# Kernel tuning notes

Measured on AMD Instinct MI355X. Metric: run time of the kernel, lower is better.

Reference implementation:

```python
import jax, jax.numpy as jnp
import numpy as np

B, DIM, HEADS, H, W = 8, 128, 8, 128, 128
EPS_NORM = 1e-12
BN_EPS = 1e-5


def _conv(x, w, b=None, pad=0, groups=1):
    # x: [N,C,H,W], w: [O, C//groups, kh, kw]
    out = jax.lax.conv_general_dilated(
        x, w, window_strides=(1, 1), padding=[(pad, pad), (pad, pad)],
        dimension_numbers=('NCHW', 'OIHW', 'NCHW'), feature_group_count=groups)
    if b is not None:
        out = out + b[None, :, None, None]
    return out


def _l2norm_lastdim(t):
    # torch F.normalize(dim=-1) semantics; works for real or complex t
    n = jnp.sqrt(jnp.sum(jnp.abs(t) ** 2, axis=-1, keepdims=True))
    return t / jnp.maximum(n, EPS_NORM)


def setup_inputs() -> dict:
    key = jax.random.key(0)
    ks = iter(jax.random.split(key, 48))
    d = DIM

    def rn(shape, scale=0.02):
        return jax.random.normal(next(ks), shape, jnp.float32) * scale

    inp = {
        'x': jax.random.normal(next(ks), (B, d, H, W), jnp.float32),
        # ---- Attention_F params ----
        'temp_f': jnp.ones((HEADS, 1, 1), jnp.float32),
        'w1': rn((d // 16, d, 1, 1)), 'b1': jnp.zeros((d // 16,), jnp.float32),
        'bn_gamma': jnp.ones((d // 16,), jnp.float32), 'bn_beta': jnp.zeros((d // 16,), jnp.float32),
        'bn_mean': jnp.zeros((d // 16,), jnp.float32), 'bn_var': jnp.ones((d // 16,), jnp.float32),
        'w2': rn((d, d // 16, 1, 1)), 'b2': jnp.zeros((d,), jnp.float32),
        'projf_w': rn((d, 2 * d, 1, 1)),
        # ---- Attention_S params ----
        'temp_s': jnp.ones((HEADS, 1, 1), jnp.float32),
        'q1_w': rn((d, d, 1, 1)), 'q1_b': jnp.zeros((d,), jnp.float32),
        'k1_w': rn((d, d, 1, 1)), 'k1_b': jnp.zeros((d,), jnp.float32),
        'v1_w': rn((d, d, 1, 1)), 'v1_b': jnp.zeros((d,), jnp.float32),
        'q3_w': rn((d // 2, 2, 3, 3)), 'q5_w': rn((d // 2, 2, 5, 5)),
        'k3_w': rn((d // 2, 2, 3, 3)), 'k5_w': rn((d // 2, 2, 5, 5)),
        'v3_w': rn((d // 2, 2, 3, 3)), 'v5_w': rn((d // 2, 2, 5, 5)),
        'c3_w': rn((d // 2, 2, 3, 3)), 'c5_w': rn((d // 2, 2, 5, 5)),
        'projs_w': rn((d, 2 * d, 1, 1)),
    }
    return inp


def _fssa(x, temp_f, w1, b1, bn_gamma, bn_beta, bn_mean, bn_var, w2, b2, projf_w,
          temp_s, q1_w, q1_b, k1_w, k1_b, v1_w, v1_b,
          q3_w, q5_w, k3_w, k5_w, v3_w, v5_w, c3_w, c5_w, projs_w):
    b, c, h, w = x.shape
    hd = c // HEADS
    groups = c // 2  # grouped convs: dim -> dim//2, 2 in-ch per group

    # ================= Attention_F (frequency branch) =================
    xf = jnp.fft.fft2(x)                     # [b,c,h,w] complex; q=k=v=fft2(x)
    qf = xf.reshape(b, HEADS, hd, h * w)
    qn = _l2norm_lastdim(qf)
    # attn: [b,head,hd,hd] complex, temperature is real [head,1,1]
    attn_f = jnp.einsum('bhcn,bhdn->bhcd', qn, qn) * temp_f[None]
    # complex softmax: softmax real & imag parts separately
    attn_f = jax.lax.complex(jax.nn.softmax(attn_f.real, axis=-1),
                             jax.nn.softmax(attn_f.imag, axis=-1))
    out_cplx = jnp.einsum('bhcd,bhdn->bhcn', attn_f, qf)
    # NOTE: torch.fft.ifft2 acts on the LAST TWO dims of [b,head,hd,hw]
    out_f = jnp.abs(jnp.fft.ifft2(out_cplx)).reshape(b, c, h, w)

    # SE-style gate in frequency domain on the real part
    g = _conv(xf.real, w1, b1)
    g = (g - bn_mean[None, :, None, None]) / jnp.sqrt(bn_var[None, :, None, None] + BN_EPS)
    g = g * bn_gamma[None, :, None, None] + bn_beta[None, :, None, None]
    g = jax.nn.relu(g)
    g = jax.nn.sigmoid(_conv(g, w2, b2))     # [b,c,h,w] real gate
    out_f_l = jnp.abs(jnp.fft.ifft2(g * xf))  # ifft2 over (h,w)

    fsa = _conv(jnp.concatenate([out_f, out_f_l], axis=1), projf_w)

    # ================= Attention_S (spatial branch) =================
    def qkv(w1x1, b1x1, w3, w5):
        t = _conv(x, w1x1, b1x1)
        return jnp.concatenate([_conv(t, w3, pad=1, groups=groups),
                                _conv(t, w5, pad=2, groups=groups)], axis=1)

    q_s = qkv(q1_w, q1_b, q3_w, q5_w).reshape(b, HEADS, hd, h * w)
    k_s = qkv(k1_w, k1_b, k3_w, k5_w).reshape(b, HEADS, hd, h * w)
    v_s = qkv(v1_w, v1_b, v3_w, v5_w).reshape(b, HEADS, hd, h * w)
    q_s = _l2norm_lastdim(q_s)
    k_s = _l2norm_lastdim(k_s)
    attn_s = jnp.einsum('bhcn,bhdn->bhcd', q_s, k_s) * temp_s[None]
    attn_s = jax.nn.softmax(attn_s, axis=-1)
    out_s = jnp.einsum('bhcd,bhdn->bhcn', attn_s, v_s).reshape(b, c, h, w)

    out_s_l = jnp.concatenate([_conv(x, c3_w, pad=1, groups=groups),
                               _conv(x, c5_w, pad=2, groups=groups)], axis=1)
    ssa = _conv(jnp.concatenate([out_s, out_s_l], axis=1), projs_w)

    return fsa + ssa


def reference(x, temp_f, w1, b1, bn_gamma, bn_beta, bn_mean, bn_var, w2, b2, projf_w,
              temp_s, q1_w, q1_b, k1_w, k1_b, v1_w, v1_b,
              q3_w, q5_w, k3_w, k5_w, v3_w, v5_w, c3_w, c5_w, projs_w):
    return _fssa(x, temp_f, w1, b1, bn_gamma, bn_beta, bn_mean, bn_var, w2, b2, projf_w,
                 temp_s, q1_w, q1_b, k1_w, k1_b, v1_w, v1_b,
                 q3_w, q5_w, k3_w, k5_w, v3_w, v5_w, c3_w, c5_w, projs_w)
```

## Files before the change

### kernel.cpp

```cpp
#include <hip/hip_runtime.h>
#include <math.h>

#define B 8
#define C 128
#define HEADS 8
#define HD 16
#define HH 128
#define WW 128
#define P 16384

static __device__ __forceinline__ float PI2F() { return 6.28318530717958647692f; }

template<int SIGN, bool GATE>
__global__ __launch_bounds__(256) void k_fftcol(
        const float* __restrict__ inR, const float* __restrict__ inI,
        const float* __restrict__ Mg, const float* __restrict__ w2,
        const float* __restrict__ b2,
        float* __restrict__ outR, float* __restrict__ outI) {
    __shared__ float2 S[128*32];
    __shared__ float2 tw[64];
    int bid = blockIdx.x;
    int img = bid >> 2;
    int qo  = (bid & 3) * 32;
    int tid = threadIdx.x;
    if (tid < 64) {
        float a = PI2F() * (float)tid / 128.0f;
        float s_, c_; __sincosf(a, &s_, &c_);
        tw[tid] = make_float2(c_, SIGN > 0 ? s_ : -s_);
    }
    long base = (long)img * P;
    float w2r[8]; float b2c = 0.f;
    const float* mb = nullptr;
    if (GATE) {
        int c = img & 127;
        #pragma unroll
        for (int j = 0; j < 8; ++j) w2r[j] = w2[c*8 + j];
        b2c = b2[c];
        mb = Mg + (long)(img >> 7)*8*P;
    }
    #pragma unroll
    for (int t = 0; t < 16; ++t) {
        int idx = tid + t*256;
        int h = idx >> 5, cc = idx & 31;
        int off = h*128 + qo + cc;
        float xr = inR[base + off];
        float xi = inI[base + off];
        if (GATE) {
            float z = b2c;
            #pragma unroll
            for (int j = 0; j < 8; ++j) z = fmaf(w2r[j], mb[(long)j*P + off], z);
            float g = 1.0f / (1.0f + __expf(-z));
            xr *= g; xi *= g;
        }
        int hr = __brev(h) >> 25;
        S[hr*32 + cc] = make_float2(xr, xi);
    }
    __syncthreads();
    int ln = tid & 31, wid = tid >> 5;
    for (int s = 0; s < 7; ++s) {
        int half = 1 << s;
        #pragma unroll
        for (int q = 0; q < 8; ++q) {
            int j = wid*8 + q;
            int k = j & (half - 1);
            int g = j >> s;
            int i0 = (g << (s+1)) + k;
            int i1 = i0 + half;
            float2 u = S[i0*32 + ln];
            float2 v = S[i1*32 + ln];
            float2 w = tw[k << (6 - s)];
            float vr = v.x*w.x - v.y*w.y;
            float vi = v.x*w.y + v.y*w.x;
            S[i0*32 + ln] = make_float2(u.x + vr, u.y + vi);
            S[i1*32 + ln] = make_float2(u.x - vr, u.y - vi);
        }
        __syncthreads();
    }
    #pragma unroll
    for (int t = 0; t < 16; ++t) {
        int idx = tid + t*256;
        int k = idx >> 5, cc = idx & 31;
        float2 z = S[k*32 + cc];
        outR[base + k*128 + qo + cc] = z.x;
        outI[base + k*128 + qo + cc] = z.y;
    }
}

template<int MODE>
__global__ __launch_bounds__(256) void k_fftrow(
        const float* __restrict__ inR, const float* __restrict__ inI,
        float* __restrict__ out, float* __restrict__ outI) {
    __shared__ float2 S[4*128];
    __shared__ float2 tw[64];
    int bid = blockIdx.x;
    int img = bid >> 5;
    int r0  = (bid & 31) * 4;
    int tid = threadIdx.x;
    if (tid < 64) {
        float a = PI2F() * (float)tid / 128.0f;
        float s_, c_; __sincosf(a, &s_, &c_);
        tw[tid] = make_float2(c_, MODE == 0 ? -s_ : s_);
    }
    long base = (long)img * P;
    #pragma unroll
    for (int t = 0; t < 2; ++t) {
        int idx = tid + t*256;
        int r = idx >> 7, w = idx & 127;
        long off = base + (long)(r0 + r)*128 + w;
        float xr = inR[off];
        float xi = (MODE == 0) ? 0.f : inI[off];
        if (MODE == 2) {
            int k2 = r0 + r;
            float ang = (PI2F()/16384.0f) * (float)(w * k2);
            float s_, c_; __sincosf(ang, &s_, &c_);
            float yr = xr*c_ - xi*s_;
            float yi = xr*s_ + xi*c_;
            xr = yr; xi = yi;
        }
        S[r*128 + (__brev(w) >> 25)] = make_float2(xr, xi);
    }
    __syncthreads();
    int r = tid >> 6, j = tid & 63;
    for (int s = 0; s < 7; ++s) {
        int half = 1 << s;
        int k = j & (half - 1);
        int g = j >> s;
        int i0 = (g << (s+1)) + k;
        int i1 = i0 + half;
        float2 u = S[r*128 + i0];
        float2 v = S[r*128 + i1];
        float2 w_ = tw[k << (6 - s)];
        float vr = v.x*w_.x - v.y*w_.y;
        float vi = v.x*w_.y + v.y*w_.x;
        S[r*128 + i0] = make_float2(u.x + vr, u.y + vi);
        S[r*128 + i1] = make_float2(u.x - vr, u.y - vi);
        __syncthreads();
    }
    if (MODE == 0) {
        #pragma unroll
        for (int t = 0; t < 2; ++t) {
            int idx = tid + t*256;
            int rr = idx >> 7, k = idx & 127;
            float2 z = S[rr*128 + k];
            long off = base + (long)(r0 + rr)*128 + k;
            out[off] = z.x; outI[off] = z.y;
        }
    } else if (MODE == 1) {
        #pragma unroll
        for (int t = 0; t < 2; ++t) {
            int idx = tid + t*256;
            int rr = idx >> 7, p = idx & 127;
            float2 z = S[rr*128 + p];
            out[base + (long)(r0 + rr)*128 + p] =
                sqrtf(z.x*z.x + z.y*z.y) * (1.0f/16384.0f);
        }
    } else {
        if (tid < 128) {
            int k1 = tid;
            float4 v;
            float2 z0 = S[0*128 + k1], z1 = S[1*128 + k1];
            float2 z2 = S[2*128 + k1], z3 = S[3*128 + k1];
            v.x = sqrtf(z0.x*z0.x + z0.y*z0.y) * (1.0f/16384.0f);
            v.y = sqrtf(z1.x*z1.x + z1.y*z1.y) * (1.0f/16384.0f);
            v.z = sqrtf(z2.x*z2.x + z2.y*z2.y) * (1.0f/16384.0f);
            v.w = sqrtf(z3.x*z3.x + z3.y*z3.y) * (1.0f/16384.0f);
            *(float4*)(out + base + (long)k1*128 + r0) = v;
        }
    }
}

__global__ __launch_bounds__(256) void k_gate_mid(
        const float* __restrict__ XFr, const float* __restrict__ w1,
        const float* __restrict__ b1, const float* __restrict__ gamma,
        const float* __restrict__ beta, const float* __restrict__ mean,
        const float* __restrict__ var, float* __restrict__ M) {
    __shared__ float w1s[8*128];
    int tid = threadIdx.x;
    for (int i = tid; i < 1024; i += 256) w1s[i] = w1[i];
    __syncthreads();
    int tile = blockIdx.x;
    int b = tile >> 4;
    long pbase = (long)(tile & 15)*1024 + tid*4;
    const float4* xp = (const float4*)(XFr + (long)b*C*P + pbase);
    float4 acc[8];
    #pragma unroll
    for (int j = 0; j < 8; ++j) { float bj = b1[j]; acc[j] = make_float4(bj,bj,bj,bj); }
    for (int c = 0; c < 128; ++c) {
        float4 xv = xp[c*(P/4)];
        #pragma unroll
        for (int j = 0; j < 8; ++j) {
            float w = w1s[j*128 + c];
            acc[j].x = fmaf(w, xv.x, acc[j].x);
            acc[j].y = fmaf(w, xv.y, acc[j].y);
            acc[j].z = fmaf(w, xv.z, acc[j].z);
            acc[j].w = fmaf(w, xv.w, acc[j].w);
        }
    }
    #pragma unroll
    for (int j = 0; j < 8; ++j) {
        float sc = rsqrtf(var[j] + 1e-5f) * gamma[j];
        float sh = beta[j] - mean[j]*sc;
        float4 v;
        v.x = fmaxf(fmaf(acc[j].x, sc, sh), 0.f);
        v.y = fmaxf(fmaf(acc[j].y, sc, sh), 0.f);
        v.z = fmaxf(fmaf(acc[j].z, sc, sh), 0.f);
        v.w = fmaxf(fmaf(acc[j].w, sc, sh), 0.f);
        *(float4*)(M + ((long)b*8 + j)*P + pbase) = v;
    }
}

__global__ __launch_bounds__(256) void k_gram_cr(
        const float* __restrict__ Xr, const float* __restrict__ Xi,
        float* __restrict__ gramP, float* __restrict__ normP) {
    __shared__ float Sr[16][260];
    __shared__ float Si[16][260];
    int bh = blockIdx.x >> 3, ck = blockIdx.x & 7;
    int tid = threadIdx.x;
    int tile = tid & 15;
    int slice = tid >> 4;
    int ci4 = (tile >> 2) * 4, di4 = (tile & 3) * 4;
    long rowb = (long)bh * 16;
    int n0 = ck * 2048;
    float acc[4][4];
    #pragma unroll
    for (int a = 0; a < 4; ++a)
        #pragma unroll
        for (int b2 = 0; b2 < 4; ++b2) acc[a][b2] = 0.f;
    float nacc = 0.f;
    int nrow = tid & 15;
    int ngrp = tid >> 4;
    for (int sc = 0; sc < 8; ++sc) {
        int nb = n0 + sc*256;
        if (sc) __syncthreads();
        for (int i = tid; i < 1024; i += 256) {
            int r = i >> 6, col = (i & 63) * 4;
            *(float4*)(&Sr[r][col]) = *(const float4*)(Xr + (rowb + r)*P + nb + col);
            *(float4*)(&Si[r][col]) = *(const float4*)(Xi + (rowb + r)*P + nb + col);
        }
        __syncthreads();
        #pragma unroll
        for (int it0 = 0; it0 < 4; ++it0) {
            int it = (it0 + slice) & 3;
            int n = slice*16 + it*4;
            float4 cr[4], cii[4], dr[4], dii[4];
            #pragma unroll
            for (int a = 0; a < 4; ++a) {
                cr[a]  = *(const float4*)(&Sr[ci4 + a][n]);
                cii[a] = *(const float4*)(&Si[ci4 + a][n]);
                dr[a]  = *(const float4*)(&Sr[di4 + a][n]);
                dii[a] = *(const float4*)(&Si[di4 + a][n]);
            }
            #pragma unroll
            for (int a = 0; a < 4; ++a)
                #pragma unroll
                for (int b2 = 0; b2 < 4; ++b2) {
                    float t = acc[a][b2];
                    t = fmaf(cr[a].x, dr[b2].x, fmaf(-cii[a].x, dii[b2].x, t));
                    t = fmaf(cr[a].y, dr[b2].y, fmaf(-cii[a].y, dii[b2].y, t));
                    t = fmaf(cr[a].z, dr[b2].z, fmaf(-cii[a].z, dii[b2].z, t));
                    t = fmaf(cr[a].w, dr[b2].w, fmaf(-cii[a].w, dii[b2].w, t));
                    acc[a][b2] = t;
                }
        }
        #pragma unroll
        for (int it0 = 0; it0 < 4; ++it0) {
            int it = (it0 + ngrp) & 3;
            int n = ngrp*16 + it*4;
            float4 r4 = *(const float4*)(&Sr[nrow][n]);
            float4 i4 = *(const float4*)(&Si[nrow][n]);
            nacc = fmaf(r4.x, r4.x, fmaf(i4.x, i4.x, nacc));
            nacc = fmaf(r4.y, r4.y, fmaf(i4.y, i4.y, nacc));
            nacc = fmaf(r4.z, r4.z, fmaf(i4.z, i4.z, nacc));
            nacc = fmaf(r4.w, r4.w, fmaf(i4.w, i4.w, nacc));
        }
    }
    __syncthreads();
    float* red  = &Sr[0][0];
    float* redn = &Si[0][0];
    #pragma unroll
    for (int a = 0; a < 4; ++a)
        #pragma unroll
        for (int b2 = 0; b2 < 4; ++b2)
            red[tile*256 + slice*16 + a*4 + b2] = acc[a][b2];
    redn[nrow*16 + ngrp] = nacc;
    __syncthreads();
    {
        int c = tid >> 4, d = tid & 15;
        int tI = (c >> 2)*4 + (d >> 2);
        int lo = (c & 3)*4 + (d & 3);
        float g = 0.f;
        #pragma unroll
        for (int s = 0; s < 16; ++s) g += red[tI*256 + s*16 + lo];
        gramP[(long)(bh*8 + ck)*256 + tid] = g;
    }
    if (tid < 16) {
        float s = 0.f;
        #pragma unroll
        for (int k = 0; k < 16; ++k) s += redn[tid*16 + k];
        normP[(long)(bh*8 + ck)*16 + tid] = s;
    }
}

__global__ __launch_bounds__(256) void k_gram_r(
        const float* __restrict__ Q, const float* __restrict__ K,
        float* __restrict__ gramP, float* __restrict__ qnormP,
        float* __restrict__ knormP) {
    __shared__ float Sq[16][260];
    __shared__ float Sk[16][260];
    int bh = blockIdx.x >> 3, ck = blockIdx.x & 7;
    int tid = threadIdx.x;
    int tile = tid & 15;
    int slice = tid >> 4;
    int ci4 = (tile >> 2) * 4, di4 = (tile & 3) * 4;
    long rowb = (long)bh * 16;
    int n0 = ck * 2048;
    float acc[4][4];
    #pragma unroll
    for (int a = 0; a < 4; ++a)
        #pragma unroll
        for (int b2 = 0; b2 < 4; ++b2) acc[a][b2] = 0.f;
    float qacc = 0.f, kacc = 0.f;
    int nrow = tid & 15, ngrp = tid >> 4;
    for (int sc = 0; sc < 8; ++sc) {
        int nb = n0 + sc*256;
        if (sc) __syncthreads();
        for (int i = tid; i < 1024; i += 256) {
            int r = i >> 6, col = (i & 63) * 4;
            *(float4*)(&Sq[r][col]) = *(const float4*)(Q + (rowb + r)*P + nb + col);
            *(float4*)(&Sk[r][col]) = *(const float4*)(K + (rowb + r)*P + nb + col);
        }
        __syncthreads();
        #pragma unroll
        for (int it0 = 0; it0 < 4; ++it0) {
            int it = (it0 + slice) & 3;
            int n = slice*16 + it*4;
            float4 cq[4], dk[4];
            #pragma unroll
            for (int a = 0; a < 4; ++a) {
                cq[a] = *(const float4*)(&Sq[ci4 + a][n]);
                dk[a] = *(const float4*)(&Sk[di4 + a][n]);
            }
            #pragma unroll
            for (int a = 0; a < 4; ++a)
                #pragma unroll
                for (int b2 = 0; b2 < 4; ++b2) {
                    float t = acc[a][b2];
                    t = fmaf(cq[a].x, dk[b2].x, t);
                    t = fmaf(cq[a].y, dk[b2].y, t);
                    t = fmaf(cq[a].z, dk[b2].z, t);
                    t = fmaf(cq[a].w, dk[b2].w, t);
                    acc[a][b2] = t;
                }
        }
        #pragma unroll
        for (int it0 = 0; it0 < 4; ++it0) {
            int it = (it0 + ngrp) & 3;
            int n = ngrp*16 + it*4;
            float4 q4 = *(const float4*)(&Sq[nrow][n]);
            float4 k4 = *(const float4*)(&Sk[nrow][n]);
            qacc = fmaf(q4.x, q4.x, qacc); kacc = fmaf(k4.x, k4.x, kacc);
            qacc = fmaf(q4.y, q4.y, qacc); kacc = fmaf(k4.y, k4.y, kacc);
            qacc = fmaf(q4.z, q4.z, qacc); kacc = fmaf(k4.z, k4.z, kacc);
            qacc = fmaf(q4.w, q4.w, qacc); kacc = fmaf(k4.w, k4.w, kacc);
        }
    }
    __syncthreads();
    float* red  = &Sq[0][0];
    float* redn = &Sk[0][0];
    #pragma unroll
    for (int a = 0; a < 4; ++a)
        #pragma unroll
        for (int b2 = 0; b2 < 4; ++b2)
            red[tile*256 + slice*16 + a*4 + b2] = acc[a][b2];
    redn[nrow*16 + ngrp] = qacc;
    redn[256 + nrow*16 + ngrp] = kacc;
    __syncthreads();
    {
        int c = tid >> 4, d = tid & 15;
        int tI = (c >> 2)*4 + (d >> 2);
        int lo = (c & 3)*4 + (d & 3);
        float g = 0.f;
        #pragma unroll
        for (int s = 0; s < 16; ++s) g += red[tI*256 + s*16 + lo];
        gramP[(long)(bh*8 + ck)*256 + tid] = g;
    }
    if (tid < 16) {
        float s = 0.f;
        #pragma unroll
        for (int k = 0; k < 16; ++k) s += redn[tid*16 + k];
        qnormP[(long)(bh*8 + ck)*16 + tid] = s;
    } else if (tid < 32) {
        int r = tid - 16;
        float s = 0.f;
        #pragma unroll
        for (int k = 0; k < 16; ++k) s += redn[256 + r*16 + k];
        knormP[(long)(bh*8 + ck)*16 + r] = s;
    }
}

__global__ void k_attn_f(const float* __restrict__ gramP, const float* __restrict__ normP,
                         const float* __restrict__ tempf, float* __restrict__ attn2) {
    int bh = blockIdx.x; int tid = threadIdx.x;
    int c = tid >> 4, d = tid & 15;
    int hh = bh & 7;
    __shared__ float sR[256];
    __shared__ float2 t16[16];
    __shared__ float sN[16];
    if (tid < 16) {
        float s = 0.f;
        #pragma unroll
        for (int ck = 0; ck < 8; ++ck) s += normP[(long)(bh*8+ck)*16 + tid];
        sN[tid] = 1.0f / fmaxf(sqrtf(s), 1e-12f);
        float a = PI2F() * (float)tid / 16.0f;
        t16[tid] = make_float2(__cosf(a), __sinf(a));
    }
    float gr = 0.f;
    for (int ck = 0; ck < 8; ++ck) gr += gramP[(long)(bh*8+ck)*256 + tid];
    __syncthreads();
    float vr = gr * sN[c] * sN[d] * tempf[hh];
    float mr = vr;
    for (int off = 8; off >= 1; off >>= 1) mr = fmaxf(mr, __shfl_xor(mr, off));
    float er = __expf(vr - mr);
    float ssr = er;
    for (int off = 8; off >= 1; off >>= 1) ssr += __shfl_xor(ssr, off);
    float arv = er / ssr;
    const float u = 1.0f/16.0f;
    sR[tid] = arv;
    __syncthreads();
    float ar2 = 0.f, ai2 = 0.f;
    #pragma unroll
    for (int cc = 0; cc < 16; ++cc) {
        float2 t = t16[(cc*c) & 15];
        float xr = sR[cc*16 + d];
        ar2 = fmaf(xr, t.x, fmaf(-u, t.y, ar2));
        ai2 = fmaf(xr, t.y, fmaf( u, t.x, ai2));
    }
    long o = ((long)bh*256 + tid)*2;
    attn2[o]   = ar2 * (1.0f/16.0f);
    attn2[o+1] = ai2 * (1.0f/16.0f);
}

__global__ void k_yf(const float* __restrict__ attn2, const float* __restrict__ Xr,
                     const float* __restrict__ Xi, float* __restrict__ Yr,
                     float* __restrict__ Yi) {
    int bh = blockIdx.x >> 6;
    int nb = blockIdx.x & 63;
    int tid = threadIdx.x;
    __shared__ float aR[256], aI[256];
    { long o = ((long)bh*256 + tid)*2; aR[tid] = attn2[o]; aI[tid] = attn2[o+1]; }
    __syncthreads();
    long n = (long)nb*256 + tid;
    long rowb = (long)bh*16;
    float qr[16], qi[16];
    #pragma unroll
    for (int dd = 0; dd < 16; ++dd) {
        qr[dd] = Xr[(rowb+dd)*P + n];
        qi[dd] = Xi[(rowb+dd)*P + n];
    }
    for (int cc = 0; cc < 16; ++cc) {
        float ar = 0.f, ai = 0.f;
        #pragma unroll
        for (int dd = 0; dd < 16; ++dd) {
            float tr = aR[cc*16+dd], ti = aI[cc*16+dd];
            ar = fmaf(tr, qr[dd], fmaf(-ti, qi[dd], ar));
            ai = fmaf(tr, qi[dd], fmaf( ti, qr[dd], ai));
        }
        Yr[(rowb+cc)*P + n] = ar;
        Yi[(rowb+cc)*P + n] = ai;
    }
}

__global__ __launch_bounds__(256) void k_conv1x1qkv(
        const float* __restrict__ x,
        const float* __restrict__ Wq, const float* __restrict__ bq,
        const float* __restrict__ Wk, const float* __restrict__ bk,
        const float* __restrict__ Wv, const float* __restrict__ bv,
        float* __restrict__ Oq, float* __restrict__ Ok,
        float* __restrict__ Ov) {
    __shared__ float Ws[16*128];
    int og = blockIdx.y & 7, which = blockIdx.y >> 3;
    int b = blockIdx.z;
    const float* W    = which == 0 ? Wq : which == 1 ? Wk : Wv;
    const float* bias = which == 0 ? bq : which == 1 ? bk : bv;
    float* O          = which == 0 ? Oq : which == 1 ? Ok : Ov;
    int tid = threadIdx.x;
    for (int i = tid; i < 2048; i += 256) Ws[i] = W[og*2048 + i];
    __syncthreads();
    long pbase = (long)blockIdx.x*1024 + tid*4;
    const float4* xp = (const float4*)(x + (long)b*C*P + pbase);
    float4 acc[16];
    #pragma unroll
    for (int j = 0; j < 16; ++j) { float bj = bias[og*16+j]; acc[j] = make_float4(bj,bj,bj,bj); }
    for (int c = 0; c < 128; ++c) {
        float4 xv = xp[c*(P/4)];
        #pragma unroll
        for (int j = 0; j < 16; ++j) {
            float w = Ws[j*128 + c];
            acc[j].x = fmaf(w, xv.x, acc[j].x);
            acc[j].y = fmaf(w, xv.y, acc[j].y);
            acc[j].z = fmaf(w, xv.z, acc[j].z);
            acc[j].w = fmaf(w, xv.w, acc[j].w);
        }
    }
    float* op = O + (long)b*C*P + (long)og*16*P + pbase;
    #pragma unroll
    for (int j = 0; j < 16; ++j) *(float4*)(op + (long)j*P) = acc[j];
}

__global__ __launch_bounds__(256) void k_gconv(
        const float* __restrict__ in, const float* __restrict__ w3,
        const float* __restrict__ w5, float* __restrict__ out) {
    __shared__ float S[2*20*132];
    __shared__ float ws3[18], ws5[50];
    int ht = blockIdx.x;
    int g  = blockIdx.y;
    int b  = blockIdx.z;
    int tid = threadIdx.x;
    int h0 = ht*16;
    const float* ib = in + ((long)b*C + 2*g)*P;
    if (tid < 18) ws3[tid] = w3[g*18 + tid];
    else if (tid < 68) ws5[tid-18] = w5[g*50 + tid - 18];
    for (int i = tid; i < 2*20*132; i += 256) {
        int ic = i / 2640, rem = i % 2640;
        int t = rem / 132, cc = rem % 132;
        int h = h0 - 2 + t, w = cc - 2;
        float v = 0.f;
        if (h >= 0 && h < 128 && w >= 0 && w < 128)
            v = ib[(long)ic*P + h*128 + w];
        S[i] = v;
    }
    __syncthreads();
    int w = tid & 127, rh = tid >> 7;
    int lr0 = rh*8;
    float acc3[8], acc5[8];
    #pragma unroll
    for (int r = 0; r < 8; ++r) { acc3[r] = 0.f; acc5[r] = 0.f; }
    #pragma unroll
    for (int ic = 0; ic < 2; ++ic) {
        const float* Sc = S + ic*2640;
        #pragma unroll
        for (int kx = 0; kx < 3; ++kx) {
            float col[10];
            #pragma unroll
            for (int i = 0; i < 10; ++i)
                col[i] = Sc[(lr0 + 1 + i)*132 + (w + 1 + kx)];
            #pragma unroll
            for (int ky = 0; ky < 3; ++ky) {
                float wv = ws3[ic*9 + ky*3 + kx];
                #pragma unroll
                for (int r = 0; r < 8; ++r)
                    acc3[r] = fmaf(wv, col[r + ky], acc3[r]);
            }
        }
        #pragma unroll
        for (int kx = 0; kx < 5; ++kx) {
            float col[12];
            #pragma unroll
            for (int i = 0; i < 12; ++i)
                col[i] = Sc[(lr0 + i)*132 + (w + kx)];
            #pragma unroll
            for (int ky = 0; ky < 5; ++ky) {
                float wv = ws5[ic*25 + ky*5 + kx];
                #pragma unroll
                for (int r = 0; r < 8; ++r)
                    acc5[r] = fmaf(wv, col[r + ky], acc5[r]);
            }
        }
    }
    long ob3 = ((long)b*C + g)*P;
    long ob5 = ((long)b*C + 64 + g)*P;
    #pragma unroll
    for (int r = 0; r < 8; ++r) {
        int h = h0 + lr0 + r;
        out[ob3 + h*128 + w] = acc3[r];
        out[ob5 + h*128 + w] = acc5[r];
    }
}

__global__ void k_attn_s(const float* __restrict__ gramP, const float* __restrict__ qnormP,
                         const float* __restrict__ knormP, const float* __restrict__ temps,
                         float* __restrict__ attn) {
    int bh = blockIdx.x; int tid = threadIdx.x;
    int c = tid >> 4, d = tid & 15;
    __shared__ float sQ[16], sK[16];
    if (tid < 16) {
        float sq = 0.f, sk = 0.f;
        #pragma unroll
        for (int ck = 0; ck < 8; ++ck) {
            sq += qnormP[(long)(bh*8+ck)*16 + tid];
            sk += knormP[(long)(bh*8+ck)*16 + tid];
        }
        sQ[tid] = 1.0f / fmaxf(sqrtf(sq), 1e-12f);
        sK[tid] = 1.0f / fmaxf(sqrtf(sk), 1e-12f);
    }
    float g = 0.f;
    for (int ck = 0; ck < 8; ++ck) g += gramP[(long)(bh*8+ck)*256 + tid];
    __syncthreads();
    g *= sQ[c] * sK[d] * temps[bh & 7];
    float m = g;
    for (int off = 8; off >= 1; off >>= 1) m = fmaxf(m, __shfl_xor(m, off));
    float e = __expf(g - m);
    float s = e;
    for (int off = 8; off >= 1; off >>= 1) s += __shfl_xor(s, off);
    attn[(long)bh*256 + tid] = e / s;
}

__global__ void k_outs(const float* __restrict__ attn, const float* __restrict__ V,
                       float* __restrict__ out) {
    int bh = blockIdx.x >> 6, nb = blockIdx.x & 63;
    int tid = threadIdx.x;
    __shared__ float aS[256];
    aS[tid] = attn[(long)bh*256 + tid];
    __syncthreads();
    long n = (long)nb*256 + tid;
    long rowb = (long)bh*16;
    float vv[16];
    #pragma unroll
    for (int dd = 0; dd < 16; ++dd) vv[dd] = V[(rowb+dd)*P + n];
    for (int cc = 0; cc < 16; ++cc) {
        float a = 0.f;
        #pragma unroll
        for (int dd = 0; dd < 16; ++dd) a = fmaf(aS[cc*16+dd], vv[dd], a);
        out[(rowb+cc)*P + n] = a;
    }
}

template<bool ADD>
__global__ __launch_bounds__(256) void k_proj2in(
        const float* __restrict__ A, const float* __restrict__ Bc,
        const float* __restrict__ W, float* __restrict__ out) {
    __shared__ float Ws[16*256];
    int og = blockIdx.y, b = blockIdx.z;
    int tid = threadIdx.x;
    for (int i = tid; i < 4096; i += 256) Ws[i] = W[og*4096 + i];
    __syncthreads();
    long pbase = (long)blockIdx.x*1024 + tid*4;
    long xb = (long)b*C*P;
    const float4* Ap = (const float4*)(A + xb + pbase);
    const float4* Bp = (const float4*)(Bc + xb + pbase);
    float4 acc[16];
    #pragma unroll
    for (int j = 0; j < 16; ++j) acc[j] = make_float4(0.f,0.f,0.f,0.f);
    for (int c = 0; c < 128; ++c) {
        float4 a = Ap[c*(P/4)];
        float4 bb = Bp[c*(P/4)];
        #pragma unroll
        for (int j = 0; j < 16; ++j) {
            float w0 = Ws[j*256 + c], w1 = Ws[j*256 + 128 + c];
            acc[j].x = fmaf(w0, a.x, fmaf(w1, bb.x, acc[j].x));
            acc[j].y = fmaf(w0, a.y, fmaf(w1, bb.y, acc[j].y));
            acc[j].z = fmaf(w0, a.z, fmaf(w1, bb.z, acc[j].z));
            acc[j].w = fmaf(w0, a.w, fmaf(w1, bb.w, acc[j].w));
        }
    }
    float* op = out + xb + (long)og*16*P + pbase;
    #pragma unroll
    for (int j = 0; j < 16; ++j) {
        float4 v = acc[j];
        if (ADD) {
            float4 o = *(float4*)(op + (long)j*P);
            v.x += o.x; v.y += o.y; v.z += o.z; v.w += o.w;
        }
        *(float4*)(op + (long)j*P) = v;
    }
}

static long ws_need_bytes(int bc) {
    long pb = (long)bc * C * P;
    long extras = (long)bc*8*P
                + (long)bc*1024*3
                + (long)bc*8*8*256
                + (long)bc*8*256*2
                + (long)bc*8*8*256
                + (long)bc*8*256;
    return (5*pb + extras) * 4;
}

extern "C" void kernel_launch(void* const* d_in, const int* in_sizes, int n_in,
                              void* d_out, int out_size, void* d_ws, size_t ws_size,
                              hipStream_t stream) {
    const float* x      = (const float*)d_in[0];
    const float* temp_f = (const float*)d_in[1];
    const float* w1     = (const float*)d_in[2];
    const float* b1     = (const float*)d_in[3];
    const float* bng    = (const float*)d_in[4];
    const float* bnb    = (const float*)d_in[5];
    const float* bnm    = (const float*)d_in[6];
    const float* bnv    = (const float*)d_in[7];
    const float* w2     = (const float*)d_in[8];
    const float* b2     = (const float*)d_in[9];
    const float* projf  = (const float*)d_in[10];
    const float* temp_s = (const float*)d_in[11];
    const float* q1w = (const float*)d_in[12]; const float* q1b = (const float*)d_in[13];
    const float* k1w = (const float*)d_in[14]; const float* k1b = (const float*)d_in[15];
    const float* v1w = (const float*)d_in[16]; const float* v1b = (const float*)d_in[17];
    const float* q3w = (const float*)d_in[18]; const float* q5w = (const float*)d_in[19];
    const float* k3w = (const float*)d_in[20]; const float* k5w = (const float*)d_in[21];
    const float* v3w = (const float*)d_in[22]; const float* v5w = (const float*)d_in[23];
    const float* c3w = (const float*)d_in[24]; const float* c5w = (const float*)d_in[25];
    const float* projs  = (const float*)d_in[26];
    float* out = (float*)d_out;
    float* ws = (float*)d_ws;

    int bc = 1;
    if ((long)ws_size >= ws_need_bytes(8)) bc = 8;
    else if ((long)ws_size >= ws_need_bytes(4)) bc = 4;
    else if ((long)ws_size >= ws_need_bytes(2)) bc = 2;
    const int NB = bc;
    const long pb = (long)bc * C * P;

    float* t0 = ws + 0*pb;
    float* t1 = ws + 1*pb;
    float* t2 = ws + 2*pb;
    float* t3 = ws + 3*pb;
    float* t4 = ws + 4*pb;
    float* Mg    = ws + 5*pb;
    float* normF = Mg + (long)bc*8*P;
    float* recQ  = normF + (long)bc*1024;
    float* recK  = recQ + (long)bc*1024;
    float* gramC = recK + (long)bc*1024;
    float* attn2 = gramC + (long)bc*8*8*256;
    float* gramS = attn2 + (long)bc*8*256*2;
    float* attnS = gramS + (long)bc*8*8*256;

    for (int ckk = 0; ckk < 8/bc; ++ckk) {
        const float* xc = x + (long)ckk * bc * C * P;
        float* outc = out + (long)ckk * bc * C * P;

        k_fftrow<0><<<NB*C*32, 256, 0, stream>>>(xc, nullptr, t0, t1);
        k_fftcol<-1,false><<<NB*C*4, 256, 0, stream>>>(t0, t1, nullptr, nullptr,
                                                       nullptr, t2, t3);
        k_gate_mid<<<NB*16, 256, 0, stream>>>(t2, w1, b1, bng, bnb, bnm, bnv, Mg);
        k_fftcol<1,true><<<NB*C*4, 256, 0, stream>>>(t2, t3, Mg, w2, b2,
                                                     t0, t1);
        k_fftrow<1><<<NB*C*32, 256, 0, stream>>>(t0, t1, t4, nullptr);
        k_gram_cr<<<NB*8*8, 256, 0, stream>>>(t2, t3, gramC, normF);
        k_attn_f<<<NB*8, 256, 0, stream>>>(gramC, normF, temp_f, attn2);
        k_yf<<<NB*8*64, 256, 0, stream>>>(attn2, t2, t3, t0, t1);
        k_fftcol<1,false><<<NB*C*4, 256, 0, stream>>>(t0, t1, nullptr, nullptr,
                                                      nullptr, t2, t3);
        k_fftrow<2><<<NB*C*32, 256, 0, stream>>>(t2, t3, t0, nullptr);
        k_proj2in<false><<<dim3(16, 8, NB), 256, 0, stream>>>(t0, t4, projf, outc);

        k_conv1x1qkv<<<dim3(16, 24, NB), 256, 0, stream>>>(xc, q1w, q1b, k1w, k1b,
                                                           v1w, v1b, t0, t1, t2);
        k_gconv<<<dim3(8, 64, NB), 256, 0, stream>>>(t0, q3w, q5w, t3);
        k_gconv<<<dim3(8, 64, NB), 256, 0, stream>>>(t1, k3w, k5w, t4);
        k_gconv<<<dim3(8, 64, NB), 256, 0, stream>>>(t2, v3w, v5w, t0);
        k_gconv<<<dim3(8, 64, NB), 256, 0, stream>>>(xc, c3w, c5w, t1);
        k_gram_r<<<NB*8*8, 256, 0, stream>>>(t3, t4, gramS, recQ, recK);
        k_attn_s<<<NB*8, 256, 0, stream>>>(gramS, recQ, recK, temp_s, attnS);
        k_outs<<<NB*8*64, 256, 0, stream>>>(attnS, t0, t2);
        k_proj2in<true><<<dim3(16, 8, NB), 256, 0, stream>>>(t2, t1, projs, outc);
    }
}
```

Measured before the change: 1.627 ms.

## Retile pointwise conv kernels with transposed smem weights and prefetch

Reworks the three 1x1-conv style kernels (gate_mid, conv1x1qkv, proj2in). Weights are stored transposed in shared memory so each channel step loads them as float4 vectors instead of scalar reads. The next channel's input is loaded one iteration early. conv1x1qkv now computes q, k and v together from a single read of x, and proj2in makes 32 outputs per thread over 2 pixels instead of 16 over 4, which halves how often each input is reread. The cost is higher register pressure from 64-96 accumulators and changed grid shapes.

```diff
diff --git a/kernel.cpp b/kernel.cpp
--- a/kernel.cpp
+++ b/kernel.cpp
@@ -10,6 +10,10 @@
 #define P 16384
 
 static __device__ __forceinline__ float PI2F() { return 6.28318530717958647692f; }
+
+#define FMA4(ACC, W, X) \
+    ACC.x = fmaf(W, X.x, ACC.x); ACC.y = fmaf(W, X.y, ACC.y); \
+    ACC.z = fmaf(W, X.z, ACC.z); ACC.w = fmaf(W, X.w, ACC.w);
 
 template<int SIGN, bool GATE>
 __global__ __launch_bounds__(256) void k_fftcol(
@@ -174,38 +178,40 @@
         const float* __restrict__ b1, const float* __restrict__ gamma,
         const float* __restrict__ beta, const float* __restrict__ mean,
         const float* __restrict__ var, float* __restrict__ M) {
-    __shared__ float w1s[8*128];
-    int tid = threadIdx.x;
-    for (int i = tid; i < 1024; i += 256) w1s[i] = w1[i];
+    __shared__ float Wt[128][8];
+    int tid = threadIdx.x;
+    for (int i = tid; i < 1024; i += 256) { int c = i >> 3, j = i & 7; Wt[c][j] = w1[j*128 + c]; }
     __syncthreads();
     int tile = blockIdx.x;
-    int b = tile >> 4;
-    long pbase = (long)(tile & 15)*1024 + tid*4;
-    const float4* xp = (const float4*)(XFr + (long)b*C*P + pbase);
-    float4 acc[8];
-    #pragma unroll
-    for (int j = 0; j < 8; ++j) { float bj = b1[j]; acc[j] = make_float4(bj,bj,bj,bj); }
+    int b = tile >> 5;
+    long pbase = (long)(tile & 31)*512 + tid*2;
+    const float2* xp = (const float2*)(XFr + (long)b*C*P + pbase);
+    float2 acc[8];
+    #pragma unroll
+    for (int j = 0; j < 8; ++j) { float bj = b1[j]; acc[j] = make_float2(bj, bj); }
+    float2 xv = xp[0];
     for (int c = 0; c < 128; ++c) {
-        float4 xv = xp[c*(P/4)];
-        #pragma unroll
-        for (int j = 0; j < 8; ++j) {
-            float w = w1s[j*128 + c];
-            acc[j].x = fmaf(w, xv.x, acc[j].x);
-            acc[j].y = fmaf(w, xv.y, acc[j].y);
-            acc[j].z = fmaf(w, xv.z, acc[j].z);
-            acc[j].w = fmaf(w, xv.w, acc[j].w);
-        }
+        float2 xn = xp[(c < 127 ? c + 1 : 127)*(P/2)];
+        const float4* wp = (const float4*)(&Wt[c][0]);
+        float4 w0 = wp[0], w1_ = wp[1];
+        acc[0].x = fmaf(w0.x, xv.x, acc[0].x); acc[0].y = fmaf(w0.x, xv.y, acc[0].y);
+        acc[1].x = fmaf(w0.y, xv.x, acc[1].x); acc[1].y = fmaf(w0.y, xv.y, acc[1].y);
+        acc[2].x = fmaf(w0.z, xv.x, acc[2].x); acc[2].y = fmaf(w0.z, xv.y, acc[2].y);
+        acc[3].x = fmaf(w0.w, xv.x, acc[3].x); acc[3].y = fmaf(w0.w, xv.y, acc[3].y);
+        acc[4].x = fmaf(w1_.x, xv.x, acc[4].x); acc[4].y = fmaf(w1_.x, xv.y, acc[4].y);
+        acc[5].x = fmaf(w1_.y, xv.x, acc[5].x); acc[5].y = fmaf(w1_.y, xv.y, acc[5].y);
+        acc[6].x = fmaf(w1_.z, xv.x, acc[6].x); acc[6].y = fmaf(w1_.z, xv.y, acc[6].y);
+        acc[7].x = fmaf(w1_.w, xv.x, acc[7].x); acc[7].y = fmaf(w1_.w, xv.y, acc[7].y);
+        xv = xn;
     }
     #pragma unroll
     for (int j = 0; j < 8; ++j) {
         float sc = rsqrtf(var[j] + 1e-5f) * gamma[j];
         float sh = beta[j] - mean[j]*sc;
-        float4 v;
+        float2 v;
         v.x = fmaxf(fmaf(acc[j].x, sc, sh), 0.f);
         v.y = fmaxf(fmaf(acc[j].y, sc, sh), 0.f);
-        v.z = fmaxf(fmaf(acc[j].z, sc, sh), 0.f);
-        v.w = fmaxf(fmaf(acc[j].w, sc, sh), 0.f);
-        *(float4*)(M + ((long)b*8 + j)*P + pbase) = v;
+        *(float2*)(M + ((long)b*8 + j)*P + pbase) = v;
     }
 }
 
@@ -477,34 +483,55 @@
         const float* __restrict__ Wv, const float* __restrict__ bv,
         float* __restrict__ Oq, float* __restrict__ Ok,
         float* __restrict__ Ov) {
-    __shared__ float Ws[16*128];
-    int og = blockIdx.y & 7, which = blockIdx.y >> 3;
+    __shared__ float Wt[128][24];
+    __shared__ float bs[24];
+    int g8 = blockIdx.y;
     int b = blockIdx.z;
-    const float* W    = which == 0 ? Wq : which == 1 ? Wk : Wv;
-    const float* bias = which == 0 ? bq : which == 1 ? bk : bv;
-    float* O          = which == 0 ? Oq : which == 1 ? Ok : Ov;
-    int tid = threadIdx.x;
-    for (int i = tid; i < 2048; i += 256) Ws[i] = W[og*2048 + i];
+    int tid = threadIdx.x;
+    for (int i = tid; i < 1024; i += 256) {
+        int c = i >> 3, j = i & 7;
+        Wt[c][j]      = Wq[(g8*8 + j)*128 + c];
+        Wt[c][8 + j]  = Wk[(g8*8 + j)*128 + c];
+        Wt[c][16 + j] = Wv[(g8*8 + j)*128 + c];
+    }
+    if (tid < 8) {
+        bs[tid]      = bq[g8*8 + tid];
+        bs[8 + tid]  = bk[g8*8 + tid];
+        bs[16 + tid] = bv[g8*8 + tid];
+    }
     __syncthreads();
     long pbase = (long)blockIdx.x*1024 + tid*4;
     const float4* xp = (const float4*)(x + (long)b*C*P + pbase);
-    float4 acc[16];
-    #pragma unroll
-    for (int j = 0; j < 16; ++j) { float bj = bias[og*16+j]; acc[j] = make_float4(bj,bj,bj,bj); }
+    float4 aq[8], ak[8], av[8];
+    #pragma unroll
+    for (int j = 0; j < 8; ++j) {
+        float v;
+        v = bs[j];      aq[j] = make_float4(v, v, v, v);
+        v = bs[8 + j];  ak[j] = make_float4(v, v, v, v);
+        v = bs[16 + j]; av[j] = make_float4(v, v, v, v);
+    }
+    float4 xv = xp[0];
     for (int c = 0; c < 128; ++c) {
-        float4 xv = xp[c*(P/4)];
-        #pragma unroll
-        for (int j = 0; j < 16; ++j) {
-            float w = Ws[j*128 + c];
-            acc[j].x = fmaf(w, xv.x, acc[j].x);
-            acc[j].y = fmaf(w, xv.y, acc[j].y);
-            acc[j].z = fmaf(w, xv.z, acc[j].z);
-            acc[j].w = fmaf(w, xv.w, acc[j].w);
-        }
-    }
-    float* op = O + (long)b*C*P + (long)og*16*P + pbase;
-    #pragma unroll
-    for (int j = 0; j < 16; ++j) *(float4*)(op + (long)j*P) = acc[j];
+        float4 xn = xp[(c < 127 ? c + 1 : 127)*(P/4)];
+        const float4* wp = (const float4*)(&Wt[c][0]);
+        float4 wq0 = wp[0], wq1 = wp[1];
+        float4 wk0 = wp[2], wk1 = wp[3];
+        float4 wv0 = wp[4], wv1 = wp[5];
+        FMA4(aq[0], wq0.x, xv) FMA4(aq[1], wq0.y, xv) FMA4(aq[2], wq0.z, xv) FMA4(aq[3], wq0.w, xv)
+        FMA4(aq[4], wq1.x, xv) FMA4(aq[5], wq1.y, xv) FMA4(aq[6], wq1.z, xv) FMA4(aq[7], wq1.w, xv)
+        FMA4(ak[0], wk0.x, xv) FMA4(ak[1], wk0.y, xv) FMA4(ak[2], wk0.z, xv) FMA4(ak[3], wk0.w, xv)
+        FMA4(ak[4], wk1.x, xv) FMA4(ak[5], wk1.y, xv) FMA4(ak[6], wk1.z, xv) FMA4(ak[7], wk1.w, xv)
+        FMA4(av[0], wv0.x, xv) FMA4(av[1], wv0.y, xv) FMA4(av[2], wv0.z, xv) FMA4(av[3], wv0.w, xv)
+        FMA4(av[4], wv1.x, xv) FMA4(av[5], wv1.y, xv) FMA4(av[6], wv1.z, xv) FMA4(av[7], wv1.w, xv)
+        xv = xn;
+    }
+    long ob = (long)b*C*P + (long)g8*8*P + pbase;
+    #pragma unroll
+    for (int j = 0; j < 8; ++j) {
+        *(float4*)(Oq + ob + (long)j*P) = aq[j];
+        *(float4*)(Ok + ob + (long)j*P) = ak[j];
+        *(float4*)(Ov + ob + (long)j*P) = av[j];
+    }
 }
 
 __global__ __launch_bounds__(256) void k_gconv(
@@ -629,39 +656,53 @@
 __global__ __launch_bounds__(256) void k_proj2in(
         const float* __restrict__ A, const float* __restrict__ Bc,
         const float* __restrict__ W, float* __restrict__ out) {
-    __shared__ float Ws[16*256];
-    int og = blockIdx.y, b = blockIdx.z;
-    int tid = threadIdx.x;
-    for (int i = tid; i < 4096; i += 256) Ws[i] = W[og*4096 + i];
-    __syncthreads();
-    long pbase = (long)blockIdx.x*1024 + tid*4;
+    __shared__ float Wt[256][32];
+    int og = blockIdx.y;
+    int b = blockIdx.z;
+    int tid = threadIdx.x;
+    for (int i = tid; i < 8192; i += 256) {
+        int c = i >> 5, j = i & 31;
+        Wt[c][j] = W[og*8192 + j*256 + c];
+    }
+    __syncthreads();
+    long pbase = (long)blockIdx.x*512 + tid*2;
     long xb = (long)b*C*P;
-    const float4* Ap = (const float4*)(A + xb + pbase);
-    const float4* Bp = (const float4*)(Bc + xb + pbase);
-    float4 acc[16];
-    #pragma unroll
-    for (int j = 0; j < 16; ++j) acc[j] = make_float4(0.f,0.f,0.f,0.f);
+    const float2* Ap = (const float2*)(A + xb + pbase);
+    const float2* Bp = (const float2*)(Bc + xb + pbase);
+    float2 acc[32];
+    #pragma unroll
+    for (int j = 0; j < 32; ++j) acc[j] = make_float2(0.f, 0.f);
+    float2 a = Ap[0], bb = Bp[0];
     for (int c = 0; c < 128; ++c) {
-        float4 a = Ap[c*(P/4)];
-        float4 bb = Bp[c*(P/4)];
-        #pragma unroll
-        for (int j = 0; j < 16; ++j) {
-            float w0 = Ws[j*256 + c], w1 = Ws[j*256 + 128 + c];
-            acc[j].x = fmaf(w0, a.x, fmaf(w1, bb.x, acc[j].x));
-            acc[j].y = fmaf(w0, a.y, fmaf(w1, bb.y, acc[j].y));
-            acc[j].z = fmaf(w0, a.z, fmaf(w1, bb.z, acc[j].z));
-            acc[j].w = fmaf(w0, a.w, fmaf(w1, bb.w, acc[j].w));
-        }
-    }
-    float* op = out + xb + (long)og*16*P + pbase;
-    #pragma unroll
-    for (int j = 0; j < 16; ++j) {
-        float4 v = acc[j];
+        int cn = (c < 127 ? c + 1 : 127);
+        float2 an = Ap[cn*(P/2)];
+        float2 bn = Bp[cn*(P/2)];
+        const float4* w0p = (const float4*)(&Wt[c][0]);
+        const float4* w1p = (const float4*)(&Wt[c + 128][0]);
+        #pragma unroll
+        for (int q = 0; q < 8; ++q) {
+            float4 w0 = w0p[q], w1 = w1p[q];
+            int j = q*4;
+            acc[j+0].x = fmaf(w0.x, a.x, fmaf(w1.x, bb.x, acc[j+0].x));
+            acc[j+0].y = fmaf(w0.x, a.y, fmaf(w1.x, bb.y, acc[j+0].y));
+            acc[j+1].x = fmaf(w0.y, a.x, fmaf(w1.y, bb.x, acc[j+1].x));
+            acc[j+1].y = fmaf(w0.y, a.y, fmaf(w1.y, bb.y, acc[j+1].y));
+            acc[j+2].x = fmaf(w0.z, a.x, fmaf(w1.z, bb.x, acc[j+2].x));
+            acc[j+2].y = fmaf(w0.z, a.y, fmaf(w1.z, bb.y, acc[j+2].y));
+            acc[j+3].x = fmaf(w0.w, a.x, fmaf(w1.w, bb.x, acc[j+3].x));
+            acc[j+3].y = fmaf(w0.w, a.y, fmaf(w1.w, bb.y, acc[j+3].y));
+        }
+        a = an; bb = bn;
+    }
+    float* op = out + xb + (long)og*32*P + pbase;
+    #pragma unroll
+    for (int j = 0; j < 32; ++j) {
+        float2 v = acc[j];
         if (ADD) {
-            float4 o = *(float4*)(op + (long)j*P);
-            v.x += o.x; v.y += o.y; v.z += o.z; v.w += o.w;
-        }
-        *(float4*)(op + (long)j*P) = v;
+            float2 o = *(float2*)(op + (long)j*P);
+            v.x += o.x; v.y += o.y;
+        }
+        *(float2*)(op + (long)j*P) = v;
     }
 }
 
@@ -730,7 +771,7 @@
         k_fftrow<0><<<NB*C*32, 256, 0, stream>>>(xc, nullptr, t0, t1);
         k_fftcol<-1,false><<<NB*C*4, 256, 0, stream>>>(t0, t1, nullptr, nullptr,
                                                        nullptr, t2, t3);
-        k_gate_mid<<<NB*16, 256, 0, stream>>>(t2, w1, b1, bng, bnb, bnm, bnv, Mg);
+        k_gate_mid<<<NB*32, 256, 0, stream>>>(t2, w1, b1, bng, bnb, bnm, bnv, Mg);
         k_fftcol<1,true><<<NB*C*4, 256, 0, stream>>>(t2, t3, Mg, w2, b2,
                                                      t0, t1);
         k_fftrow<1><<<NB*C*32, 256, 0, stream>>>(t0, t1, t4, nullptr);
@@ -740,9 +781,9 @@
         k_fftcol<1,false><<<NB*C*4, 256, 0, stream>>>(t0, t1, nullptr, nullptr,
                                                       nullptr, t2, t3);
         k_fftrow<2><<<NB*C*32, 256, 0, stream>>>(t2, t3, t0, nullptr);
-        k_proj2in<false><<<dim3(16, 8, NB), 256, 0, stream>>>(t0, t4, projf, outc);
-
-        k_conv1x1qkv<<<dim3(16, 24, NB), 256, 0, stream>>>(xc, q1w, q1b, k1w, k1b,
+        k_proj2in<false><<<dim3(32, 4, NB), 256, 0, stream>>>(t0, t4, projf, outc);
+
+        k_conv1x1qkv<<<dim3(16, 16, NB), 256, 0, stream>>>(xc, q1w, q1b, k1w, k1b,
                                                            v1w, v1b, t0, t1, t2);
         k_gconv<<<dim3(8, 64, NB), 256, 0, stream>>>(t0, q3w, q5w, t3);
         k_gconv<<<dim3(8, 64, NB), 256, 0, stream>>>(t1, k3w, k5w, t4);
@@ -751,6 +792,6 @@
         k_gram_r<<<NB*8*8, 256, 0, stream>>>(t3, t4, gramS, recQ, recK);
         k_attn_s<<<NB*8, 256, 0, stream>>>(gramS, recQ, recK, temp_s, attnS);
         k_outs<<<NB*8*64, 256, 0, stream>>>(attnS, t0, t2);
-        k_proj2in<true><<<dim3(16, 8, NB), 256, 0, stream>>>(t2, t1, projs, outc);
-    }
-}
+        k_proj2in<true><<<dim3(32, 4, NB), 256, 0, stream>>>(t2, t1, projs, outc);
+    }
+}
```

New measurement: 1.549 ms. 1.05x faster.
